# Performance work log

Measured on AMD Instinct MI355X. Metric: run time of the kernel, lower is better.

The kernel has to match this reference:

```python
import jax, jax.numpy as jnp
import numpy as np

EMBED_DIM = 1024
K_DIM = 64
NUM_HEADS = 16


def setup_inputs() -> dict:
    key = jax.random.key(0)
    kx, kq, kk, kv, kw = jax.random.split(key, 5)
    x = jax.random.normal(kx, (4, 2048, EMBED_DIM), dtype=jnp.float32)
    # per-head weights stacked along a leading head axis (torch.randn init)
    wq = jax.random.normal(kq, (NUM_HEADS, EMBED_DIM, K_DIM), dtype=jnp.float32)
    wk = jax.random.normal(kk, (NUM_HEADS, EMBED_DIM, K_DIM), dtype=jnp.float32)
    wv = jax.random.normal(kv, (NUM_HEADS, EMBED_DIM, K_DIM), dtype=jnp.float32)
    w = jax.random.normal(kw, (NUM_HEADS * K_DIM, EMBED_DIM), dtype=jnp.float32)
    return {"x": x, "wq": wq, "wk": wk, "wv": wv, "w": w}


def reference(x, wq, wk, wv, w):
    # x: [B,S,D]; wq/wk/wv: [H,D,K]; w: [H*K, D]
    q = jnp.einsum('bsd,hdk->bhsk', x, wq)
    k = jnp.einsum('bsd,hdk->bhsk', x, wk)
    v = jnp.einsum('bsd,hdk->bhsk', x, wv)
    scale = 1.0 / jnp.sqrt(jnp.asarray(K_DIM, x.dtype))
    scores = jnp.einsum('bhsk,bhtk->bhst', q, k) * scale  # [B,H,S,S]
    attn = jax.nn.softmax(scores, axis=-1)
    ctx = jnp.einsum('bhst,bhtk->bhsk', attn, v)  # [B,H,S,K]
    B, H, S, K = ctx.shape
    # concat heads along last dim in head order (matches torch.cat of per-head outs)
    heads = jnp.transpose(ctx, (0, 2, 1, 3)).reshape(B, S, H * K)
    return jnp.matmul(heads, w)  # [B,S,D]
```

## Files before the change

kernel.cpp:

```cpp
#include <hip/hip_runtime.h>
#include <hip/hip_bf16.h>
#include <math.h>

#define EMBED 1024
#define KD 64
#define NH 16
#define SEQ 2048
#define BATCH 4
#define BH (BATCH * NH)
#define NTOK ((size_t)BH * SEQ * KD)

typedef float4 f4;
typedef unsigned short u16;
typedef __attribute__((ext_vector_type(8))) short v8s;
typedef __attribute__((ext_vector_type(4))) float v4f;

__device__ __forceinline__ u16 f2bf(float f) {
    unsigned u = __float_as_uint(f);
    unsigned r = (u + 0x7fffu + ((u >> 16) & 1u)) >> 16;
    return (u16)r;
}
__device__ __forceinline__ float bf2f(u16 h) {
    return __uint_as_float(((unsigned)h) << 16);
}

__device__ __forceinline__ void gload_lds16(const void* g, void* l) {
    __builtin_amdgcn_global_load_lds(
        (const __attribute__((address_space(1))) unsigned int*)g,
        (__attribute__((address_space(3))) unsigned int*)l, 16, 0, 0);
}

__global__ __launch_bounds__(256)
void convert_all_kernel(const float* __restrict__ x,
                        const float* __restrict__ wq, const float* __restrict__ wk,
                        const float* __restrict__ wv, const float* __restrict__ w,
                        u16* __restrict__ xh, u16* __restrict__ xl,
                        u16* __restrict__ Wth, u16* __restrict__ Wtl,
                        u16* __restrict__ OWth, u16* __restrict__ OWtl)
{
    int b = blockIdx.x;
    if (b < 8192) {
        size_t i = ((size_t)b * 256 + threadIdx.x) * 4;
        f4 v = *(const f4*)(x + i);
        u16 h0 = f2bf(v.x), h1 = f2bf(v.y), h2 = f2bf(v.z), h3 = f2bf(v.w);
        u16 l0 = f2bf(v.x - bf2f(h0)), l1 = f2bf(v.y - bf2f(h1));
        u16 l2 = f2bf(v.z - bf2f(h2)), l3 = f2bf(v.w - bf2f(h3));
        uint2 H, L;
        H.x = (unsigned)h0 | ((unsigned)h1 << 16);
        H.y = (unsigned)h2 | ((unsigned)h3 << 16);
        L.x = (unsigned)l0 | ((unsigned)l1 << 16);
        L.y = (unsigned)l2 | ((unsigned)l3 << 16);
        *(uint2*)(xh + i) = H;
        *(uint2*)(xl + i) = L;
    } else if (b < 8192 + 3072) {
        int n = b - 8192;
        int mat = n >> 10, nin = n & 1023, h = nin >> 6, c = nin & 63;
        const float* __restrict__ ws = (mat == 0) ? wq : (mat == 1) ? wk : wv;
        float sc = (mat == 0) ? (0.125f * 1.4426950408889634f) : 1.0f;
        for (int d = threadIdx.x; d < EMBED; d += 256) {
            float f = ws[((size_t)h * EMBED + d) * KD + c] * sc;
            u16 hi = f2bf(f);
            u16 lo = f2bf(f - bf2f(hi));
            Wth[(size_t)n * EMBED + d] = hi;
            Wtl[(size_t)n * EMBED + d] = lo;
        }
    } else {
        int n = b - 11264;
        for (int k = threadIdx.x; k < EMBED; k += 256) {
            float f = w[(size_t)k * EMBED + n];
            u16 hi = f2bf(f);
            u16 lo = f2bf(f - bf2f(hi));
            OWth[(size_t)n * EMBED + k] = hi;
            OWtl[(size_t)n * EMBED + k] = lo;
        }
    }
}

__global__ __launch_bounds__(256)
void qkv_mfma_kernel(const u16* __restrict__ xh, const u16* __restrict__ xl,
                     const u16* __restrict__ Wth, const u16* __restrict__ Wtl,
                     u16* __restrict__ Qhi, u16* __restrict__ Qlo,
                     u16* __restrict__ Khi, u16* __restrict__ Klo,
                     u16* __restrict__ Vt)
{
    __shared__ u16 sAh[128 * 64];
    __shared__ u16 sAl[128 * 64];
    __shared__ u16 sBh[128 * 64];
    __shared__ u16 sBl[128 * 64];
    const int tid = threadIdx.x;
    const int lane = tid & 63, wid = tid >> 6;
    const int lm = lane & 15, lq = lane >> 4;
    const int wm = wid & 1, wn = wid >> 1;
    const int m0 = blockIdx.y * 128;
    const int n0 = blockIdx.x * 128;
    const bool three = (n0 < 2048);

    v4f acc[4][4];
#pragma unroll
    for (int mt = 0; mt < 4; ++mt)
#pragma unroll
        for (int nt = 0; nt < 4; ++nt)
            acc[mt][nt] = (v4f){0.f, 0.f, 0.f, 0.f};

    const int srow = wid * 32 + (lane >> 3);
    const int sblk = (lane & 7) ^ (lane >> 3);

    for (int k0 = 0; k0 < EMBED; k0 += 64) {
        __syncthreads();
#pragma unroll
        for (int i = 0; i < 4; ++i) {
            int row = srow + i * 8;
            size_t gA = (((size_t)(m0 + row)) << 10) + k0 + sblk * 8;
            size_t gB = (((size_t)(n0 + row)) << 10) + k0 + sblk * 8;
            int lo = (wid * 32 + i * 8) * 128;
            gload_lds16((const char*)xh + gA * 2, (char*)sAh + lo);
            gload_lds16((const char*)Wth + gB * 2, (char*)sBh + lo);
            if (three) {
                gload_lds16((const char*)xl + gA * 2, (char*)sAl + lo);
                gload_lds16((const char*)Wtl + gB * 2, (char*)sBl + lo);
            }
        }
        asm volatile("s_waitcnt vmcnt(0)" ::: "memory");
        __syncthreads();

#pragma unroll
        for (int kks = 0; kks < 2; ++kks) {
            v8s ah[4], bh[4];
            const int ba = ((kks * 4 + lq) ^ (lm & 7)) * 8;
#pragma unroll
            for (int t = 0; t < 4; ++t) {
                int ra = wm * 64 + t * 16 + lm;
                int rb = wn * 64 + t * 16 + lm;
                ah[t] = *(const v8s*)&sAh[ra * 64 + ba];
                bh[t] = *(const v8s*)&sBh[rb * 64 + ba];
            }
            if (three) {
                v8s al[4], bl[4];
#pragma unroll
                for (int t = 0; t < 4; ++t) {
                    int ra = wm * 64 + t * 16 + lm;
                    int rb = wn * 64 + t * 16 + lm;
                    al[t] = *(const v8s*)&sAl[ra * 64 + ba];
                    bl[t] = *(const v8s*)&sBl[rb * 64 + ba];
                }
#pragma unroll
                for (int mt = 0; mt < 4; ++mt)
#pragma unroll
                    for (int nt = 0; nt < 4; ++nt) {
                        acc[mt][nt] = __builtin_amdgcn_mfma_f32_16x16x32_bf16(ah[mt], bh[nt], acc[mt][nt], 0, 0, 0);
                        acc[mt][nt] = __builtin_amdgcn_mfma_f32_16x16x32_bf16(ah[mt], bl[nt], acc[mt][nt], 0, 0, 0);
                        acc[mt][nt] = __builtin_amdgcn_mfma_f32_16x16x32_bf16(al[mt], bh[nt], acc[mt][nt], 0, 0, 0);
                    }
            } else {
#pragma unroll
                for (int mt = 0; mt < 4; ++mt)
#pragma unroll
                    for (int nt = 0; nt < 4; ++nt)
                        acc[mt][nt] = __builtin_amdgcn_mfma_f32_16x16x32_bf16(ah[mt], bh[nt], acc[mt][nt], 0, 0, 0);
            }
        }
    }

    const int mrow0 = m0 + wm * 64;
    const int ncol0 = n0 + wn * 64;
    if (!three) {
#pragma unroll
        for (int mt = 0; mt < 4; ++mt) {
            int sbase = mrow0 + mt * 16 + lq * 4;
            int bb = sbase >> 11, s = sbase & 2047;
#pragma unroll
            for (int nt = 0; nt < 4; ++nt) {
                int nin = (ncol0 + nt * 16 + lm) & 1023;
                int h = nin >> 6, cc = nin & 63;
                int bh_ = bb * NH + h;
                size_t a = ((size_t)bh_ * KD + cc) * SEQ
                         + (size_t)(((((s >> 3) ^ (cc & 7)) << 3)) | (s & 7));
                uint2 u;
                u.x = (unsigned)f2bf(acc[mt][nt][0]) | ((unsigned)f2bf(acc[mt][nt][1]) << 16);
                u.y = (unsigned)f2bf(acc[mt][nt][2]) | ((unsigned)f2bf(acc[mt][nt][3]) << 16);
                *(uint2*)(Vt + a) = u;
            }
        }
    } else {
        const bool isQ = (n0 < 1024);
#pragma unroll
        for (int mt = 0; mt < 4; ++mt) {
            int sbase = mrow0 + mt * 16 + lq * 4;
            int bb = sbase >> 11, sB = sbase & 2047;
#pragma unroll
            for (int nt = 0; nt < 4; ++nt) {
                int nin = (ncol0 + nt * 16 + lm) & 1023;
                int h = nin >> 6, cc = nin & 63;
                int bh_ = bb * NH + h;
#pragma unroll
                for (int r = 0; r < 4; ++r) {
                    int s = sB + r;
                    float f = acc[mt][nt][r];
                    u16 hi = f2bf(f);
                    u16 lo = f2bf(f - bf2f(hi));
                    if (isQ) {
                        size_t a = ((size_t)bh_ * SEQ + s) * KD + cc;
                        Qhi[a] = hi;
                        Qlo[a] = lo;
                    } else {
                        int ccp = ((((cc >> 3) ^ (s & 7)) << 3) | (cc & 7));
                        size_t a = ((size_t)bh_ * SEQ + s) * KD + ccp;
                        Khi[a] = hi;
                        Klo[a] = lo;
                    }
                }
            }
        }
    }
}

__global__ __launch_bounds__(256)
void attn_kernel(const u16* __restrict__ Qhi, const u16* __restrict__ Qlo,
                 const u16* __restrict__ Khi, const u16* __restrict__ Klo,
                 const u16* __restrict__ Vt,  u16* __restrict__ headsb)
{
    __shared__ u16 sKhi[64 * 64];
    __shared__ u16 sKlo[64 * 64];
    __shared__ u16 sVt[64 * 64];
    __shared__ u16 sPs[128 * 64];

    const int tid = threadIdx.x;
    const int lane = tid & 63, wid = tid >> 6;
    const int lm = lane & 15, lq = lane >> 4;
    const int psw = (lm & 7) << 3;
    const int q0 = blockIdx.x * 128;
    const int bh = blockIdx.y;
    const int bb = bh >> 4, h = bh & 15;

    v8s qh[2][2], ql[2][2];
#pragma unroll
    for (int qt = 0; qt < 2; ++qt)
#pragma unroll
        for (int kk = 0; kk < 2; ++kk) {
            size_t g = ((size_t)bh * SEQ + q0 + wid * 32 + qt * 16 + lm) * KD
                     + kk * 32 + lq * 8;
            qh[qt][kk] = *(const v8s*)(Qhi + g);
            ql[qt][kk] = *(const v8s*)(Qlo + g);
        }

    v8s vones;
#pragma unroll
    for (int i = 0; i < 8; ++i) vones[i] = (short)0x3F80;

    int bpaddr[4];
#pragma unroll
    for (int r = 0; r < 4; ++r)
        bpaddr[r] = (((lane & 48) | (lq * 4 + r)) << 2);

    v4f ctx[2][4], lcol[2];
    float mrun[2];
#pragma unroll
    for (int qt = 0; qt < 2; ++qt) {
        lcol[qt] = (v4f){0.f, 0.f, 0.f, 0.f};
        mrun[qt] = -INFINITY;
#pragma unroll
        for (int nt = 0; nt < 4; ++nt)
            ctx[qt][nt] = (v4f){0.f, 0.f, 0.f, 0.f};
    }

    const size_t kbase = (size_t)bh * SEQ * KD;

    for (int t0 = 0; t0 < SEQ; t0 += 64) {
        __syncthreads();
        {
            const char* gk1 = (const char*)(Khi + kbase + (size_t)t0 * KD);
            const char* gk2 = (const char*)(Klo + kbase + (size_t)t0 * KD);
            int off = wid * 2048;
#pragma unroll
            for (int i = 0; i < 2; ++i) {
                int o = off + i * 1024;
                gload_lds16(gk1 + o + lane * 16, (char*)sKhi + o);
                gload_lds16(gk2 + o + lane * 16, (char*)sKlo + o);
            }
        }
#pragma unroll
        for (int i = 0; i < 2; ++i) {
            int row = wid * 16 + i * 8;
            const char* gv = (const char*)(Vt + ((size_t)bh * KD + row + (lane >> 3)) * SEQ + t0)
                           + (lane & 7) * 16;
            gload_lds16(gv, (char*)sVt + row * 128);
        }
        asm volatile("s_waitcnt vmcnt(0)" ::: "memory");
        __syncthreads();

        v4f sc[4][2];
#pragma unroll
        for (int kt = 0; kt < 4; ++kt)
#pragma unroll
            for (int qt = 0; qt < 2; ++qt)
                sc[kt][qt] = (v4f){0.f, 0.f, 0.f, 0.f};
        __builtin_amdgcn_s_setprio(1);
#pragma unroll
        for (int kk = 0; kk < 2; ++kk) {
#pragma unroll
            for (int kt = 0; kt < 4; ++kt) {
                int key = kt * 16 + lm;
                int blk = (kk * 4 + lq) ^ (key & 7);
                v8s kh16 = *(const v8s*)&sKhi[key * 64 + blk * 8];
                v8s kl16 = *(const v8s*)&sKlo[key * 64 + blk * 8];
#pragma unroll
                for (int qt = 0; qt < 2; ++qt) {
                    sc[kt][qt] = __builtin_amdgcn_mfma_f32_16x16x32_bf16(kh16, qh[qt][kk], sc[kt][qt], 0, 0, 0);
                    sc[kt][qt] = __builtin_amdgcn_mfma_f32_16x16x32_bf16(kl16, qh[qt][kk], sc[kt][qt], 0, 0, 0);
                    sc[kt][qt] = __builtin_amdgcn_mfma_f32_16x16x32_bf16(kh16, ql[qt][kk], sc[kt][qt], 0, 0, 0);
                }
            }
        }
        __builtin_amdgcn_s_setprio(0);

        float aq[2];
#pragma unroll
        for (int qt = 0; qt < 2; ++qt) {
            float m0v = fmaxf(fmaxf(fmaxf(sc[0][qt][0], sc[0][qt][1]), sc[0][qt][2]), sc[0][qt][3]);
            float m1v = fmaxf(fmaxf(fmaxf(sc[1][qt][0], sc[1][qt][1]), sc[1][qt][2]), sc[1][qt][3]);
            float m2v = fmaxf(fmaxf(fmaxf(sc[2][qt][0], sc[2][qt][1]), sc[2][qt][2]), sc[2][qt][3]);
            float m3v = fmaxf(fmaxf(fmaxf(sc[3][qt][0], sc[3][qt][1]), sc[3][qt][2]), sc[3][qt][3]);
            float mx = fmaxf(fmaxf(fmaxf(m0v, m1v), m2v), m3v);
            mx = fmaxf(mx, __shfl_xor(mx, 16));
            mx = fmaxf(mx, __shfl_xor(mx, 32));
            float mold = mrun[qt];
            float mnew = fmaxf(mold, mx);
            aq[qt] = __builtin_amdgcn_exp2f(mold - mnew);
            mrun[qt] = mnew;
            u16* pbase = &sPs[(wid * 32 + qt * 16 + lm) * 64];
#pragma unroll
            for (int kt = 0; kt < 4; ++kt) {
                unsigned u0 = __float_as_uint(__builtin_amdgcn_exp2f(sc[kt][qt][0] - mnew));
                unsigned u1 = __float_as_uint(__builtin_amdgcn_exp2f(sc[kt][qt][1] - mnew));
                unsigned u2 = __float_as_uint(__builtin_amdgcn_exp2f(sc[kt][qt][2] - mnew));
                unsigned u3 = __float_as_uint(__builtin_amdgcn_exp2f(sc[kt][qt][3] - mnew));
                uint2 pk;
                pk.x = __builtin_amdgcn_perm(u1, u0, 0x07060302);
                pk.y = __builtin_amdgcn_perm(u3, u2, 0x07060302);
                *(uint2*)&pbase[(kt * 16 + lq * 4) ^ psw] = pk;
            }
        }

#pragma unroll
        for (int qt = 0; qt < 2; ++qt) {
#pragma unroll
            for (int r = 0; r < 4; ++r) {
                float ar = __uint_as_float(
                    __builtin_amdgcn_ds_bpermute(bpaddr[r], __float_as_uint(aq[qt])));
                lcol[qt][r] *= ar;
#pragma unroll
                for (int nt = 0; nt < 4; ++nt)
                    ctx[qt][nt][r] *= ar;
            }
        }

        __builtin_amdgcn_s_setprio(1);
#pragma unroll
        for (int kk2 = 0; kk2 < 2; ++kk2) {
            v8s a[2];
#pragma unroll
            for (int qt = 0; qt < 2; ++qt)
                a[qt] = *(const v8s*)&sPs[(wid * 32 + qt * 16 + lm) * 64 + ((kk2 * 32 + lq * 8) ^ psw)];
#pragma unroll
            for (int nt = 0; nt < 4; ++nt) {
                int hd = nt * 16 + lm;
                int blk = (kk2 * 4 + lq) ^ (hd & 7);
                v8s b = *(const v8s*)&sVt[hd * 64 + blk * 8];
#pragma unroll
                for (int qt = 0; qt < 2; ++qt)
                    ctx[qt][nt] = __builtin_amdgcn_mfma_f32_16x16x32_bf16(a[qt], b, ctx[qt][nt], 0, 0, 0);
            }
#pragma unroll
            for (int qt = 0; qt < 2; ++qt)
                lcol[qt] = __builtin_amdgcn_mfma_f32_16x16x32_bf16(a[qt], vones, lcol[qt], 0, 0, 0);
        }
        __builtin_amdgcn_s_setprio(0);
    }

#pragma unroll
    for (int qt = 0; qt < 2; ++qt)
#pragma unroll
        for (int r = 0; r < 4; ++r) {
            int row = q0 + wid * 32 + qt * 16 + lq * 4 + r;
            float inv = 1.0f / lcol[qt][r];
            u16* dst = headsb + ((size_t)bb * SEQ + row) * EMBED + h * KD;
#pragma unroll
            for (int nt = 0; nt < 4; ++nt)
                dst[nt * 16 + lm] = f2bf(ctx[qt][nt][r] * inv);
        }
}

__global__ __launch_bounds__(256)
void out_mfma_kernel(const u16* __restrict__ headsb,
                     const u16* __restrict__ OWth, const u16* __restrict__ OWtl,
                     float* __restrict__ out)
{
    __shared__ u16 sA[128 * 64];
    __shared__ u16 sBh[128 * 64];
    __shared__ u16 sBl[128 * 64];
    const int tid = threadIdx.x;
    const int lane = tid & 63, wid = tid >> 6;
    const int lm = lane & 15, lq = lane >> 4;
    const int wm = wid & 1, wn = wid >> 1;
    const int m0 = blockIdx.y * 128;
    const int n0 = blockIdx.x * 128;

    v4f acc[4][4];
#pragma unroll
    for (int mt = 0; mt < 4; ++mt)
#pragma unroll
        for (int nt = 0; nt < 4; ++nt)
            acc[mt][nt] = (v4f){0.f, 0.f, 0.f, 0.f};

    const int srow = wid * 32 + (lane >> 3);
    const int sblk = (lane & 7) ^ (lane >> 3);

    for (int k0 = 0; k0 < EMBED; k0 += 64) {
        __syncthreads();
#pragma unroll
        for (int i = 0; i < 4; ++i) {
            int row = srow + i * 8;
            size_t gA = (((size_t)(m0 + row)) << 10) + k0 + sblk * 8;
            size_t gB = (((size_t)(n0 + row)) << 10) + k0 + sblk * 8;
            int lo = (wid * 32 + i * 8) * 128;
            gload_lds16((const char*)headsb + gA * 2, (char*)sA + lo);
            gload_lds16((const char*)OWth + gB * 2, (char*)sBh + lo);
            gload_lds16((const char*)OWtl + gB * 2, (char*)sBl + lo);
        }
        asm volatile("s_waitcnt vmcnt(0)" ::: "memory");
        __syncthreads();

#pragma unroll
        for (int kks = 0; kks < 2; ++kks) {
            const int ba = ((kks * 4 + lq) ^ (lm & 7)) * 8;
            v8s ah[4], bh[4], bl[4];
#pragma unroll
            for (int t = 0; t < 4; ++t) {
                int ra = wm * 64 + t * 16 + lm;
                int rb = wn * 64 + t * 16 + lm;
                ah[t] = *(const v8s*)&sA[ra * 64 + ba];
                bh[t] = *(const v8s*)&sBh[rb * 64 + ba];
                bl[t] = *(const v8s*)&sBl[rb * 64 + ba];
            }
#pragma unroll
            for (int mt = 0; mt < 4; ++mt)
#pragma unroll
                for (int nt = 0; nt < 4; ++nt) {
                    acc[mt][nt] = __builtin_amdgcn_mfma_f32_16x16x32_bf16(ah[mt], bh[nt], acc[mt][nt], 0, 0, 0);
                    acc[mt][nt] = __builtin_amdgcn_mfma_f32_16x16x32_bf16(ah[mt], bl[nt], acc[mt][nt], 0, 0, 0);
                }
        }
    }

    const int mrow0 = m0 + wm * 64;
    const int ncol0 = n0 + wn * 64;
#pragma unroll
    for (int mt = 0; mt < 4; ++mt) {
        int sbase = mrow0 + mt * 16 + lq * 4;
#pragma unroll
        for (int nt = 0; nt < 4; ++nt) {
            int n = ncol0 + nt * 16 + lm;
#pragma unroll
            for (int r = 0; r < 4; ++r)
                out[(size_t)(sbase + r) * EMBED + n] = acc[mt][nt][r];
        }
    }
}

extern "C" void kernel_launch(void* const* d_in, const int* in_sizes, int n_in,
                              void* d_out, int out_size, void* d_ws, size_t ws_size,
                              hipStream_t stream) {
    const float* x  = (const float*)d_in[0];
    const float* wq = (const float*)d_in[1];
    const float* wk = (const float*)d_in[2];
    const float* wv = (const float*)d_in[3];
    const float* w  = (const float*)d_in[4];
    float* out = (float*)d_out;

    u16* Qhi = (u16*)d_ws;
    u16* Qlo = Qhi + NTOK;
    u16* Khi = Qlo + NTOK;
    u16* Klo = Khi + NTOK;
    u16* Vt  = Klo + NTOK;
    u16* xh  = Vt + NTOK;
    u16* xl  = xh + NTOK;
    u16* Wth = xl + NTOK;
    u16* Wtl = Wth + (size_t)3072 * 1024;
    u16* OWth = Wtl + (size_t)3072 * 1024;
    u16* OWtl = OWth + (size_t)1024 * 1024;
    u16* headsb = xh;

    convert_all_kernel<<<12288, 256, 0, stream>>>(x, wq, wk, wv, w,
                                                  xh, xl, Wth, Wtl, OWth, OWtl);

    dim3 g1(24, 64);
    qkv_mfma_kernel<<<g1, 256, 0, stream>>>(xh, xl, Wth, Wtl, Qhi, Qlo, Khi, Klo, Vt);

    dim3 g2(SEQ / 128, BH);
    attn_kernel<<<g2, 256, 0, stream>>>(Qhi, Qlo, Khi, Klo, Vt, headsb);

    dim3 g3(8, 64);
    out_mfma_kernel<<<g3, 256, 0, stream>>>(headsb, OWth, OWtl, out);
}
```

Measured before the change: 421.7 us.

## Register-prefetch next K/V tile, skip lazy softmax rescale, swap grid axes

The attention kernel stops using direct global-to-LDS loads with a full vmcnt wait each iteration. It now prefetches the next K/V tile into registers while the current tile is computed, then stores it to LDS at the top of the next iteration. It also adds a lazy online-softmax rescale that updates the running max and rescales the accumulators only when some row's tile max exceeds the running max by more than 8 (log2 domain). The grid axes are swapped so consecutive blocks work on different heads rather than different query tiles of the same head, which changes L2 locality for K/V. The trade-off is more registers and VGPR-to-LDS store traffic, and a stale max bounds exp2 outputs by 2^8, which should stay within fp32 range.

```diff
diff --git a/kernel.cpp b/kernel.cpp
--- a/kernel.cpp
+++ b/kernel.cpp
@@ -228,8 +228,8 @@
     const int lane = tid & 63, wid = tid >> 6;
     const int lm = lane & 15, lq = lane >> 4;
     const int psw = (lm & 7) << 3;
-    const int q0 = blockIdx.x * 128;
-    const int bh = blockIdx.y;
+    const int q0 = blockIdx.y * 128;
+    const int bh = blockIdx.x;
     const int bb = bh >> 4, h = bh & 15;
 
     v8s qh[2][2], ql[2][2];
@@ -265,27 +265,42 @@
 
     const size_t kbase = (size_t)bh * SEQ * KD;
 
+    const char* gKh = (const char*)(Khi + kbase);
+    const char* gKl = (const char*)(Klo + kbase);
+    const int ko1 = wid * 2048 + lane * 16;
+    const int ko2 = ko1 + 1024;
+    const int vrow0 = wid * 16 + (lane >> 3);
+    const char* gV0 = (const char*)(Vt + ((size_t)bh * KD + vrow0) * SEQ) + (lane & 7) * 16;
+    const char* gV1 = (const char*)(Vt + ((size_t)bh * KD + vrow0 + 8) * SEQ) + (lane & 7) * 16;
+
+    f4 rk0, rk1, rl0, rl1, rv0, rv1;
+    {
+        rk0 = *(const f4*)(gKh + ko1);
+        rk1 = *(const f4*)(gKh + ko2);
+        rl0 = *(const f4*)(gKl + ko1);
+        rl1 = *(const f4*)(gKl + ko2);
+        rv0 = *(const f4*)(gV0);
+        rv1 = *(const f4*)(gV1);
+    }
+
     for (int t0 = 0; t0 < SEQ; t0 += 64) {
         __syncthreads();
-        {
-            const char* gk1 = (const char*)(Khi + kbase + (size_t)t0 * KD);
-            const char* gk2 = (const char*)(Klo + kbase + (size_t)t0 * KD);
-            int off = wid * 2048;
-#pragma unroll
-            for (int i = 0; i < 2; ++i) {
-                int o = off + i * 1024;
-                gload_lds16(gk1 + o + lane * 16, (char*)sKhi + o);
-                gload_lds16(gk2 + o + lane * 16, (char*)sKlo + o);
-            }
-        }
-#pragma unroll
-        for (int i = 0; i < 2; ++i) {
-            int row = wid * 16 + i * 8;
-            const char* gv = (const char*)(Vt + ((size_t)bh * KD + row + (lane >> 3)) * SEQ + t0)
-                           + (lane & 7) * 16;
-            gload_lds16(gv, (char*)sVt + row * 128);
-        }
-        asm volatile("s_waitcnt vmcnt(0)" ::: "memory");
+        *(f4*)((char*)sKhi + ko1) = rk0;
+        *(f4*)((char*)sKhi + ko2) = rk1;
+        *(f4*)((char*)sKlo + ko1) = rl0;
+        *(f4*)((char*)sKlo + ko2) = rl1;
+        *(f4*)((char*)sVt  + ko1) = rv0;
+        *(f4*)((char*)sVt  + ko2) = rv1;
+        if (t0 + 64 < SEQ) {
+            size_t tb = (size_t)(t0 + 64) * 128;
+            size_t vb = (size_t)(t0 + 64) * 2;
+            rk0 = *(const f4*)(gKh + tb + ko1);
+            rk1 = *(const f4*)(gKh + tb + ko2);
+            rl0 = *(const f4*)(gKl + tb + ko1);
+            rl1 = *(const f4*)(gKl + tb + ko2);
+            rv0 = *(const f4*)(gV0 + vb);
+            rv1 = *(const f4*)(gV1 + vb);
+        }
         __syncthreads();
 
         v4f sc[4][2];
@@ -313,20 +328,39 @@
         }
         __builtin_amdgcn_s_setprio(0);
 
-        float aq[2];
+        float mx[2];
 #pragma unroll
         for (int qt = 0; qt < 2; ++qt) {
             float m0v = fmaxf(fmaxf(fmaxf(sc[0][qt][0], sc[0][qt][1]), sc[0][qt][2]), sc[0][qt][3]);
             float m1v = fmaxf(fmaxf(fmaxf(sc[1][qt][0], sc[1][qt][1]), sc[1][qt][2]), sc[1][qt][3]);
             float m2v = fmaxf(fmaxf(fmaxf(sc[2][qt][0], sc[2][qt][1]), sc[2][qt][2]), sc[2][qt][3]);
             float m3v = fmaxf(fmaxf(fmaxf(sc[3][qt][0], sc[3][qt][1]), sc[3][qt][2]), sc[3][qt][3]);
-            float mx = fmaxf(fmaxf(fmaxf(m0v, m1v), m2v), m3v);
-            mx = fmaxf(mx, __shfl_xor(mx, 16));
-            mx = fmaxf(mx, __shfl_xor(mx, 32));
-            float mold = mrun[qt];
-            float mnew = fmaxf(mold, mx);
-            aq[qt] = __builtin_amdgcn_exp2f(mold - mnew);
-            mrun[qt] = mnew;
+            float v = fmaxf(fmaxf(fmaxf(m0v, m1v), m2v), m3v);
+            v = fmaxf(v, __shfl_xor(v, 16));
+            v = fmaxf(v, __shfl_xor(v, 32));
+            mx[qt] = v;
+        }
+        if (!__all((int)((mx[0] <= mrun[0] + 8.f) && (mx[1] <= mrun[1] + 8.f)))) {
+#pragma unroll
+            for (int qt = 0; qt < 2; ++qt) {
+                float mold = mrun[qt];
+                float mnew = fmaxf(mold, mx[qt]);
+                float a = __builtin_amdgcn_exp2f(mold - mnew);
+                mrun[qt] = mnew;
+#pragma unroll
+                for (int r = 0; r < 4; ++r) {
+                    float ar = __uint_as_float(
+                        __builtin_amdgcn_ds_bpermute(bpaddr[r], __float_as_uint(a)));
+                    lcol[qt][r] *= ar;
+#pragma unroll
+                    for (int nt = 0; nt < 4; ++nt)
+                        ctx[qt][nt][r] *= ar;
+                }
+            }
+        }
+#pragma unroll
+        for (int qt = 0; qt < 2; ++qt) {
+            float mnew = mrun[qt];
             u16* pbase = &sPs[(wid * 32 + qt * 16 + lm) * 64];
 #pragma unroll
             for (int kt = 0; kt < 4; ++kt) {
@@ -338,19 +372,6 @@
                 pk.x = __builtin_amdgcn_perm(u1, u0, 0x07060302);
                 pk.y = __builtin_amdgcn_perm(u3, u2, 0x07060302);
                 *(uint2*)&pbase[(kt * 16 + lq * 4) ^ psw] = pk;
-            }
-        }
-
-#pragma unroll
-        for (int qt = 0; qt < 2; ++qt) {
-#pragma unroll
-            for (int r = 0; r < 4; ++r) {
-                float ar = __uint_as_float(
-                    __builtin_amdgcn_ds_bpermute(bpaddr[r], __float_as_uint(aq[qt])));
-                lcol[qt][r] *= ar;
-#pragma unroll
-                for (int nt = 0; nt < 4; ++nt)
-                    ctx[qt][nt][r] *= ar;
             }
         }
 
@@ -496,7 +517,7 @@
     dim3 g1(24, 64);
     qkv_mfma_kernel<<<g1, 256, 0, stream>>>(xh, xl, Wth, Wtl, Qhi, Qlo, Khi, Klo, Vt);
 
-    dim3 g2(SEQ / 128, BH);
+    dim3 g2(BH, SEQ / 128);
     attn_kernel<<<g2, 256, 0, stream>>>(Qhi, Qlo, Khi, Klo, Vt, headsb);
 
     dim3 g3(8, 64);
```

Measured after the change: 445.2 us. 1.06x slower.
